# Optimization experiments

Hardware: AMD Instinct MI355X
Metric: run time of the kernel (lower is better)

## Reference

```python
import jax, jax.numpy as jnp
import numpy as np

S = 2048          # total tokens (single sequence)
H = 2560          # hidden size
NH = 8            # query heads
NKV = 4           # kv heads
D = 256           # head dim
EPS = 1e-6
SCALING = 256.0 ** -0.5          # query_pre_attn_scalar ** -0.5
WINDOW = 1024 - 1                # config.sliding_window - 1
ROPE_THETA = 10000.0             # rope_local_base_freq (sliding layer)


def setup_inputs() -> dict:
    key = jax.random.key(0)
    ks = jax.random.split(key, 5)
    hidden_states = jax.random.normal(ks[0], (S, H), dtype=jnp.float32)
    # RoPE tables (default rope type, HF convention: freqs duplicated along last dim)
    inv_freq = 1.0 / (ROPE_THETA ** (np.arange(0, D, 2, dtype=np.float32) / D))
    pos = np.arange(S, dtype=np.float32)
    freqs = np.outer(pos, inv_freq)                 # [S, D/2]
    emb = np.concatenate([freqs, freqs], axis=-1)   # [S, D]
    cos = jnp.asarray(np.cos(emb), dtype=jnp.float32)
    sin = jnp.asarray(np.sin(emb), dtype=jnp.float32)
    w_qkv = jax.random.normal(ks[1], (H, (NH + 2 * NKV) * D), dtype=jnp.float32) * (H ** -0.5)
    w_o = jax.random.normal(ks[2], (NH * D, H), dtype=jnp.float32) * ((NH * D) ** -0.5)
    q_norm_w = jax.random.normal(ks[3], (D,), dtype=jnp.float32) * 0.02
    k_norm_w = jax.random.normal(ks[4], (D,), dtype=jnp.float32) * 0.02
    return {"hidden_states": hidden_states, "cos": cos, "sin": sin,
            "w_qkv": w_qkv, "w_o": w_o, "q_norm_w": q_norm_w, "k_norm_w": k_norm_w}


def _rms_norm(x, w):
    # Gemma3RMSNorm: x * rsqrt(mean(x^2)+eps) * (1 + w), computed in fp32
    var = jnp.mean(jnp.square(x), axis=-1, keepdims=True)
    return x * jax.lax.rsqrt(var + EPS) * (1.0 + w)


def _rotate_half(x):
    x1, x2 = jnp.split(x, 2, axis=-1)
    return jnp.concatenate([-x2, x1], axis=-1)


def reference(hidden_states, cos, sin, w_qkv, w_o, q_norm_w, k_norm_w):
    qkv = hidden_states @ w_qkv                          # [S, (NH+2NKV)*D]
    q, k, v = jnp.split(qkv, [NH * D, (NH + NKV) * D], axis=-1)
    q = q.reshape(S, NH, D)
    k = k.reshape(S, NKV, D)
    v = v.reshape(S, NKV, D)

    # per-head QK RMSNorm
    q = _rms_norm(q, q_norm_w)
    k = _rms_norm(k, k_norm_w)

    # RoPE (cos/sin broadcast over heads)
    c = cos[:, None, :]
    s = sin[:, None, :]
    q = q * c + _rotate_half(q) * s
    k = k * c + _rotate_half(k) * s

    # GQA expand kv heads
    rep = NH // NKV
    k = jnp.repeat(k, rep, axis=1)                       # [S, NH, D]
    v = jnp.repeat(v, rep, axis=1)

    scores = jnp.einsum('snd,tnd->nst', q, k) * SCALING  # [NH, S, S]
    i = jnp.arange(S)[:, None]
    j = jnp.arange(S)[None, :]
    allowed = (j <= i) & (i - j <= WINDOW)               # causal sliding window
    scores = jnp.where(allowed[None], scores, jnp.finfo(scores.dtype).min)
    probs = jax.nn.softmax(scores, axis=-1)
    attn = jnp.einsum('nst,tnd->snd', probs, v)          # [S, NH, D]
    out = attn.reshape(S, NH * D) @ w_o                  # [S, H]
    return out
```

## Files before the change

### kernel.cpp

```cpp
#include <hip/hip_runtime.h>
#include <hip/hip_bf16.h>
#include <cstdint>
#include <cstddef>

#define S_LEN 2048
#define HID   2560
#define NHQ   8
#define QKV_N 4096
#define ATT_N 2048
#define WIN   1023
#define SCALE 0.0625f
#define NINF  -3.0e38f

typedef __attribute__((ext_vector_type(8))) short bf16x8;
typedef __attribute__((ext_vector_type(4))) float f32x4;

__device__ __forceinline__ unsigned bf_hi(float f) {
  unsigned u = __builtin_bit_cast(unsigned, f);
  return (u + 0x7FFFu + ((u >> 16) & 1u)) >> 16;
}
__device__ __forceinline__ float bf_to_f(unsigned h) {
  return __builtin_bit_cast(float, h << 16);
}
__device__ __forceinline__ void g2l16(const void* g, void* l) {
  __builtin_amdgcn_global_load_lds((const __attribute__((address_space(1))) void*)g,
                                   (__attribute__((address_space(3))) void*)l,
                                   16, 0, 0);
}

__global__ __launch_bounds__(256) void split_rows(const float* __restrict__ X,
                                                  unsigned short* __restrict__ Xh,
                                                  unsigned short* __restrict__ Xl) {
  const size_t i = ((size_t)blockIdx.x * 256 + threadIdx.x) * 8;
  const float4 v0 = *(const float4*)(X + i);
  const float4 v1 = *(const float4*)(X + i + 4);
  const float f[8] = {v0.x, v0.y, v0.z, v0.w, v1.x, v1.y, v1.z, v1.w};
  unsigned hw[4], lw[4];
  #pragma unroll
  for (int j = 0; j < 4; ++j) {
    const unsigned h0 = bf_hi(f[2 * j]), h1 = bf_hi(f[2 * j + 1]);
    const float r0 = f[2 * j] - bf_to_f(h0), r1 = f[2 * j + 1] - bf_to_f(h1);
    hw[j] = h0 | (h1 << 16);
    lw[j] = bf_hi(r0) | (bf_hi(r1) << 16);
  }
  *(uint4*)(Xh + i) = make_uint4(hw[0], hw[1], hw[2], hw[3]);
  *(uint4*)(Xl + i) = make_uint4(lw[0], lw[1], lw[2], lw[3]);
}

__global__ __launch_bounds__(256) void split_transpose(const float* __restrict__ W,
                                                       unsigned short* __restrict__ Th,
                                                       unsigned short* __restrict__ Tl,
                                                       int K, int N) {
  __shared__ float tile[32][33];
  const int tid = threadIdx.x;
  const int kt = blockIdx.y * 32, nt = blockIdx.x * 32;
  {
    const int r = tid >> 3, c = (tid & 7) * 4;
    const float4 v = *(const float4*)(W + (size_t)(kt + r) * N + nt + c);
    tile[r][c] = v.x; tile[r][c + 1] = v.y; tile[r][c + 2] = v.z; tile[r][c + 3] = v.w;
  }
  __syncthreads();
  const int nl = tid >> 3, k = (tid & 7) * 4;
  unsigned hw[2], lw[2];
  #pragma unroll
  for (int j = 0; j < 2; ++j) {
    const float f0 = tile[k + 2 * j][nl], f1 = tile[k + 2 * j + 1][nl];
    const unsigned h0 = bf_hi(f0), h1 = bf_hi(f1);
    const float r0 = f0 - bf_to_f(h0), r1 = f1 - bf_to_f(h1);
    hw[j] = h0 | (h1 << 16);
    lw[j] = bf_hi(r0) | (bf_hi(r1) << 16);
  }
  *(uint2*)(Th + (size_t)(nt + nl) * K + kt + k) = make_uint2(hw[0], hw[1]);
  *(uint2*)(Tl + (size_t)(nt + nl) * K + kt + k) = make_uint2(lw[0], lw[1]);
}

__global__ __launch_bounds__(256) void gemm_bf16_split(
    const unsigned short* __restrict__ Ah, const unsigned short* __restrict__ Al,
    const unsigned short* __restrict__ Bh, const unsigned short* __restrict__ Bl,
    float* __restrict__ C, int M, int N, int K, int nbx) {
  __shared__ __align__(16) unsigned short smem[16384];

  const int tid = threadIdx.x;
  int bid = blockIdx.x;
  const int cpx = gridDim.x >> 3;
  bid = (bid & 7) * cpx + (bid >> 3);
  const int bm = (bid / nbx) * 128;
  const int bn = (bid % nbx) * 128;

  const int lane = tid & 63;
  const int wv = tid >> 6;
  const int wr = (wv >> 1) * 64;
  const int wc = (wv & 1) * 64;
  const int frow = lane & 15;
  const int g16 = lane >> 4;

  const int u0 = tid, u1 = tid + 256;
  const int r0 = u0 >> 2, s0 = (u0 & 3) ^ ((r0 >> 1) & 3);
  const int r1 = u1 >> 2, s1 = (u1 & 3) ^ ((r1 >> 1) & 3);

  const unsigned short* a_h = Ah + (size_t)bm * K;
  const unsigned short* a_l = Al + (size_t)bm * K;
  const unsigned short* b_h = Bh + (size_t)bn * K;
  const unsigned short* b_l = Bl + (size_t)bn * K;

  unsigned short* d0 = smem + ((tid & ~63) << 3);
  unsigned short* d1 = smem + 2048 + ((tid & ~63) << 3);

  const int sx = (g16 ^ ((frow >> 1) & 3)) * 8;

  f32x4 acc[4][4] = {};

  for (int k0 = 0; k0 < K; k0 += 32) {
    __syncthreads();
    {
      const size_t o0 = (size_t)r0 * K + k0 + s0 * 8;
      const size_t o1 = (size_t)r1 * K + k0 + s1 * 8;
      g2l16(a_h + o0, d0);
      g2l16(a_h + o1, d1);
      g2l16(a_l + o0, d0 + 4096);
      g2l16(a_l + o1, d1 + 4096);
      g2l16(b_h + o0, d0 + 8192);
      g2l16(b_h + o1, d1 + 8192);
      g2l16(b_l + o0, d0 + 12288);
      g2l16(b_l + o1, d1 + 12288);
    }
    __syncthreads();

    bf16x8 ah[4], al[4], bh[4], bl[4];
    #pragma unroll
    for (int i = 0; i < 4; ++i) {
      ah[i] = *(const bf16x8*)&smem[(wr + i * 16 + frow) * 32 + sx];
      al[i] = *(const bf16x8*)&smem[4096 + (wr + i * 16 + frow) * 32 + sx];
      bh[i] = *(const bf16x8*)&smem[8192 + (wc + i * 16 + frow) * 32 + sx];
      bl[i] = *(const bf16x8*)&smem[12288 + (wc + i * 16 + frow) * 32 + sx];
    }
    #pragma unroll
    for (int i = 0; i < 4; ++i)
      #pragma unroll
      for (int j = 0; j < 4; ++j) {
        acc[i][j] = __builtin_amdgcn_mfma_f32_16x16x32_bf16(ah[i], bh[j], acc[i][j], 0, 0, 0);
        acc[i][j] = __builtin_amdgcn_mfma_f32_16x16x32_bf16(ah[i], bl[j], acc[i][j], 0, 0, 0);
        acc[i][j] = __builtin_amdgcn_mfma_f32_16x16x32_bf16(al[i], bh[j], acc[i][j], 0, 0, 0);
      }
  }

  #pragma unroll
  for (int i = 0; i < 4; ++i) {
    const int row0 = bm + wr + i * 16 + g16 * 4;
    #pragma unroll
    for (int j = 0; j < 4; ++j) {
      const int c = bn + wc + j * 16 + frow;
      #pragma unroll
      for (int r = 0; r < 4; ++r)
        C[(size_t)(row0 + r) * N + c] = acc[i][j][r];
    }
  }
}

__global__ __launch_bounds__(256) void qk_norm_rope_split(
    const float* __restrict__ qkv, const float* __restrict__ cosp,
    const float* __restrict__ sinp, const float* __restrict__ qw,
    const float* __restrict__ kw,
    unsigned short* __restrict__ Qh, unsigned short* __restrict__ Ql,
    unsigned short* __restrict__ Kh, unsigned short* __restrict__ Kl) {
  const int lane = threadIdx.x & 63;
  const int wave = threadIdx.x >> 6;
  const int row  = blockIdx.x * 4 + wave;
  const int s    = row / 12;
  const int c    = row % 12;
  const float* p = qkv + (size_t)s * QKV_N + c * 256;

  float4 x = *(const float4*)(p + lane * 4);
  float ss = x.x * x.x + x.y * x.y + x.z * x.z + x.w * x.w;
  #pragma unroll
  for (int off = 32; off; off >>= 1) ss += __shfl_xor(ss, off);
  const float scale = rsqrtf(ss * (1.0f / 256.0f) + 1e-6f);

  const float* wp = (c < 8) ? qw : kw;
  float4 w4 = *(const float4*)(wp + lane * 4);
  float y0 = x.x * scale * (1.0f + w4.x);
  float y1 = x.y * scale * (1.0f + w4.y);
  float y2 = x.z * scale * (1.0f + w4.z);
  float y3 = x.w * scale * (1.0f + w4.w);

  float z0 = __shfl_xor(y0, 32);
  float z1 = __shfl_xor(y1, 32);
  float z2 = __shfl_xor(y2, 32);
  float z3 = __shfl_xor(y3, 32);
  const float sgn = (lane < 32) ? -1.0f : 1.0f;

  float4 c4 = *(const float4*)(cosp + (size_t)s * 256 + lane * 4);
  float4 s4 = *(const float4*)(sinp + (size_t)s * 256 + lane * 4);
  float o[4];
  o[0] = y0 * c4.x + sgn * z0 * s4.x;
  o[1] = y1 * c4.y + sgn * z1 * s4.y;
  o[2] = y2 * c4.z + sgn * z2 * s4.z;
  o[3] = y3 * c4.w + sgn * z3 * s4.w;

  const float mul = (c < 8) ? SCALE : 1.0f;
  #pragma unroll
  for (int j = 0; j < 4; ++j) o[j] *= mul;

  unsigned h[4], lo[4];
  #pragma unroll
  for (int j = 0; j < 4; ++j) {
    h[j] = bf_hi(o[j]);
    lo[j] = bf_hi(o[j] - bf_to_f(h[j]));
  }
  const size_t off = ((c < 8) ? ((size_t)c * S_LEN + s)
                              : ((size_t)(c - 8) * S_LEN + s)) * 256 + lane * 4;
  unsigned short* dh = (c < 8 ? Qh : Kh) + off;
  unsigned short* dl = (c < 8 ? Ql : Kl) + off;
  *(uint2*)dh = make_uint2(h[0] | (h[1] << 16), h[2] | (h[3] << 16));
  *(uint2*)dl = make_uint2(lo[0] | (lo[1] << 16), lo[2] | (lo[3] << 16));
}

__global__ __launch_bounds__(256) void v_split_transpose(
    const float* __restrict__ qkv,
    unsigned short* __restrict__ VTh, unsigned short* __restrict__ VTl) {
  __shared__ float tile[32][33];
  const int tid = threadIdx.x;
  const int s0 = blockIdx.x * 32, d0 = blockIdx.y * 32, kvh = blockIdx.z;
  {
    const int r = tid >> 3, c = (tid & 7) * 4;
    const float4 v = *(const float4*)(qkv + (size_t)(s0 + r) * QKV_N + 3072 + kvh * 256 + d0 + c);
    tile[r][c] = v.x; tile[r][c + 1] = v.y; tile[r][c + 2] = v.z; tile[r][c + 3] = v.w;
  }
  __syncthreads();
  const int dd = tid >> 3, sc = (tid & 7) * 4;
  unsigned h[4], lo[4];
  #pragma unroll
  for (int j = 0; j < 4; ++j) {
    const float f = tile[sc + j][dd];
    h[j] = bf_hi(f);
    lo[j] = bf_hi(f - bf_to_f(h[j]));
  }
  const size_t off = ((size_t)kvh * 256 + d0 + dd) * S_LEN + s0 + sc;
  *(uint2*)(VTh + off) = make_uint2(h[0] | (h[1] << 16), h[2] | (h[3] << 16));
  *(uint2*)(VTl + off) = make_uint2(lo[0] | (lo[1] << 16), lo[2] | (lo[3] << 16));
}

#define PH_U  32768
#define PL_U  34048
__global__ __launch_bounds__(128, 2) void attn_mfma(
    const unsigned short* __restrict__ Qh, const unsigned short* __restrict__ Ql,
    const unsigned short* __restrict__ Kh, const unsigned short* __restrict__ Kl,
    const unsigned short* __restrict__ VTh, const unsigned short* __restrict__ VTl,
    unsigned short* __restrict__ Oh, unsigned short* __restrict__ Ol) {
  __shared__ __align__(16) unsigned short smem[35328];

  const int tid  = threadIdx.x;
  const int lane = tid & 63;
  const int wv   = __builtin_amdgcn_readfirstlane(tid >> 6);
  const int b    = blockIdx.x;
  const int xcd  = b & 7;
  const int kvh  = xcd >> 1;
  const int head = kvh * 2 + ((b >> 3) & 1);
  const int q0   = (((b >> 4) << 1) | (xcd & 1)) * 32;
  const int g16  = lane >> 4;
  const int c16  = lane & 15;

  const int qrow = q0 + wv * 16 + c16;
  bf16x8 qh[8], ql[8];
  {
    const unsigned short* qph = Qh + ((size_t)head * S_LEN + qrow) * 256 + g16 * 8;
    const unsigned short* qpl = Ql + ((size_t)head * S_LEN + qrow) * 256 + g16 * 8;
    #pragma unroll
    for (int dc = 0; dc < 8; ++dc) {
      qh[dc] = *(const bf16x8*)(qph + dc * 32);
      ql[dc] = *(const bf16x8*)(qpl + dc * 32);
    }
  }

  f32x4 o_acc[16] = {};
  float m_run[4], l_run[4];
  #pragma unroll
  for (int r = 0; r < 4; ++r) { m_run[r] = NINF; l_run[r] = 0.0f; }

  const int rmin = q0 + wv * 16, rmax = rmin + 15;
  const unsigned short* kh_g  = Kh  + (size_t)kvh * S_LEN * 256;
  const unsigned short* kl_g  = Kl  + (size_t)kvh * S_LEN * 256;
  const unsigned short* vth_g = VTh + (size_t)kvh * 256 * S_LEN;
  const unsigned short* vtl_g = VTl + (size_t)kvh * 256 * S_LEN;

  const int kstart = (q0 > WIN) ? ((q0 - WIN) & ~31) : 0;
  const int kend   = q0 + 31;

  for (int t0 = kstart; t0 <= kend; t0 += 32) {
    {
      char* lbase = (char*)smem + ((tid & ~63) << 4);
      #pragma unroll
      for (int i = 0; i < 8; ++i) {
        const int uu = i * 128 + tid, row = uu >> 5, sl = uu & 31;
        g2l16(kh_g + (size_t)(t0 + row) * 256 + ((sl ^ (row & 7)) * 8),
              lbase + i * 2048);
      }
      #pragma unroll
      for (int i = 0; i < 8; ++i) {
        const int uu = i * 128 + tid, row = uu >> 5, sl = uu & 31;
        g2l16(kl_g + (size_t)(t0 + row) * 256 + ((sl ^ (row & 7)) * 8),
              lbase + 16384 + i * 2048);
      }
      #pragma unroll
      for (int i = 0; i < 8; ++i) {
        const int uu = i * 128 + tid, d = uu >> 2, sl = uu & 3;
        g2l16(vth_g + (size_t)d * S_LEN + t0 + ((sl ^ ((d >> 1) & 3)) * 8),
              lbase + 32768 + i * 2048);
      }
      #pragma unroll
      for (int i = 0; i < 8; ++i) {
        const int uu = i * 128 + tid, d = uu >> 2, sl = uu & 3;
        g2l16(vtl_g + (size_t)d * S_LEN + t0 + ((sl ^ ((d >> 1) & 3)) * 8),
              lbase + 49152 + i * 2048);
      }
    }
    __syncthreads();

    const bool active = (t0 <= rmax) && (t0 + 31 + WIN >= rmin);
    if (active) {
      f32x4 sa[2] = {};
      #pragma unroll
      for (int t = 0; t < 2; ++t) {
        const int krow = t * 16 + c16;
        const int swz = krow & 7;
        #pragma unroll
        for (int dc = 0; dc < 8; ++dc) {
          const int sl = ((dc * 4 + g16) ^ swz) * 16;
          const bf16x8 kfh = *(const bf16x8*)((const char*)smem + krow * 512 + sl);
          const bf16x8 kfl = *(const bf16x8*)((const char*)smem + 16384 + krow * 512 + sl);
          sa[t] = __builtin_amdgcn_mfma_f32_16x16x32_bf16(qh[dc], kfh, sa[t], 0, 0, 0);
          sa[t] = __builtin_amdgcn_mfma_f32_16x16x32_bf16(qh[dc], kfl, sa[t], 0, 0, 0);
          sa[t] = __builtin_amdgcn_mfma_f32_16x16x32_bf16(ql[dc], kfh, sa[t], 0, 0, 0);
        }
      }

      const int k0c = t0 + c16;
      #pragma unroll
      for (int r = 0; r < 4; ++r) {
        const int q = rmin + g16 * 4 + r;
        const bool v0 = (k0c <= q) && (q - k0c <= WIN);
        const bool v1 = (k0c + 16 <= q) && (q - (k0c + 16) <= WIN);
        float s0 = v0 ? sa[0][r] : NINF;
        float s1 = v1 ? sa[1][r] : NINF;
        float mx = fmaxf(s0, s1);
        #pragma unroll
        for (int off = 8; off; off >>= 1) mx = fmaxf(mx, __shfl_xor(mx, off));
        const float m_new = fmaxf(m_run[r], mx);
        const float rs = __expf(m_run[r] - m_new);
        const float p0 = v0 ? __expf(s0 - m_new) : 0.0f;
        const float p1 = v1 ? __expf(s1 - m_new) : 0.0f;
        float psum = p0 + p1;
        #pragma unroll
        for (int off = 8; off; off >>= 1) psum += __shfl_xor(psum, off);
        l_run[r] = l_run[r] * rs + psum;
        m_run[r] = m_new;
        #pragma unroll
        for (int dt = 0; dt < 16; ++dt) o_acc[dt][r] *= rs;
        const int pro = wv * 640 + (g16 * 4 + r) * 40;
        const unsigned h0 = bf_hi(p0), h1 = bf_hi(p1);
        smem[PH_U + pro + c16]      = (unsigned short)h0;
        smem[PH_U + pro + 16 + c16] = (unsigned short)h1;
        smem[PL_U + pro + c16]      = (unsigned short)bf_hi(p0 - bf_to_f(h0));
        smem[PL_U + pro + 16 + c16] = (unsigned short)bf_hi(p1 - bf_to_f(h1));
      }

      const bf16x8 pah = *(const bf16x8*)&smem[PH_U + wv * 640 + c16 * 40 + g16 * 8];
      const bf16x8 pal = *(const bf16x8*)&smem[PL_U + wv * 640 + c16 * 40 + g16 * 8];
      #pragma unroll
      for (int dt = 0; dt < 16; ++dt) {
        const int vrow = dt * 16 + c16;
        const int sl = (g16 ^ ((vrow >> 1) & 3)) * 16;
        const bf16x8 vfh = *(const bf16x8*)((const char*)smem + 32768 + vrow * 64 + sl);
        const bf16x8 vfl = *(const bf16x8*)((const char*)smem + 49152 + vrow * 64 + sl);
        o_acc[dt] = __builtin_amdgcn_mfma_f32_16x16x32_bf16(pah, vfh, o_acc[dt], 0, 0, 0);
        o_acc[dt] = __builtin_amdgcn_mfma_f32_16x16x32_bf16(pah, vfl, o_acc[dt], 0, 0, 0);
        o_acc[dt] = __builtin_amdgcn_mfma_f32_16x16x32_bf16(pal, vfh, o_acc[dt], 0, 0, 0);
      }
    }
    __syncthreads();
  }

  #pragma unroll
  for (int r = 0; r < 4; ++r) {
    const float inv = 1.0f / l_run[r];
    const size_t rowo = (size_t)(rmin + g16 * 4 + r) * ATT_N + head * 256 + c16;
    #pragma unroll
    for (int dt = 0; dt < 16; ++dt) {
      const float o = o_acc[dt][r] * inv;
      const unsigned h = bf_hi(o);
      Oh[rowo + dt * 16] = (unsigned short)h;
      Ol[rowo + dt * 16] = (unsigned short)bf_hi(o - bf_to_f(h));
    }
  }
}

extern "C" void kernel_launch(void* const* d_in, const int* in_sizes, int n_in,
                              void* d_out, int out_size, void* d_ws, size_t ws_size,
                              hipStream_t stream) {
  const float* hs    = (const float*)d_in[0];
  const float* cosp  = (const float*)d_in[1];
  const float* sinp  = (const float*)d_in[2];
  const float* w_qkv = (const float*)d_in[3];
  const float* w_o   = (const float*)d_in[4];
  const float* qw    = (const float*)d_in[5];
  const float* kw    = (const float*)d_in[6];

  const size_t MB = 1024 * 1024;
  char* ws = (char*)d_ws;
  float* qkv = (float*)ws;
  unsigned short* wh = (unsigned short*)(ws + 32 * MB);
  unsigned short* wl = (unsigned short*)(ws + 52 * MB);
  unsigned short* Qh = (unsigned short*)(ws + 32 * MB);
  unsigned short* Ql = (unsigned short*)(ws + 40 * MB);
  unsigned short* Kh = (unsigned short*)(ws + 48 * MB);
  unsigned short* Kl = (unsigned short*)(ws + 52 * MB);
  unsigned short* VTh = (unsigned short*)(ws + 56 * MB);
  unsigned short* VTl = (unsigned short*)(ws + 60 * MB);
  unsigned short* Oh = (unsigned short*)ws;
  unsigned short* Ol = (unsigned short*)(ws + 8 * MB);
  unsigned short* oh = (unsigned short*)(ws + 16 * MB);
  unsigned short* ol = (unsigned short*)(ws + 26 * MB);
  unsigned short* Ahs = (unsigned short*)d_out;
  unsigned short* Als = Ahs + (size_t)S_LEN * HID;
  float* out = (float*)d_out;

  split_rows<<<(S_LEN * HID) / (256 * 8), 256, 0, stream>>>(hs, Ahs, Als);
  split_transpose<<<dim3(QKV_N / 32, HID / 32), 256, 0, stream>>>(
      w_qkv, wh, wl, HID, QKV_N);
  gemm_bf16_split<<<(S_LEN / 128) * (QKV_N / 128), 256, 0, stream>>>(
      Ahs, Als, wh, wl, qkv, S_LEN, QKV_N, HID, QKV_N / 128);
  qk_norm_rope_split<<<(S_LEN * 12) / 4, 256, 0, stream>>>(
      qkv, cosp, sinp, qw, kw, Qh, Ql, Kh, Kl);
  v_split_transpose<<<dim3(S_LEN / 32, 256 / 32, 4), 256, 0, stream>>>(
      qkv, VTh, VTl);
  attn_mfma<<<512, 128, 0, stream>>>(Qh, Ql, Kh, Kl, VTh, VTl, Oh, Ol);
  split_transpose<<<dim3(HID / 32, ATT_N / 32), 256, 0, stream>>>(
      w_o, oh, ol, ATT_N, HID);
  gemm_bf16_split<<<(S_LEN / 128) * (HID / 128), 256, 0, stream>>>(
      Oh, Ol, oh, ol, out, S_LEN, HID, ATT_N, HID / 128);
}
```

Measured before the change: 502.4 us.

## Split attention KV range in two partitions with a separate combine kernel

Attention is split into single-wave blocks of 16 query rows. Each block handles half of the key tiles for its query tile and writes unnormalised fp32 partial outputs plus running max and sum. A new combine kernel merges the two partials and emits the hi/lo bf16 split output. K and V fragments are now read straight from global memory instead of being staged through shared memory. This is meant to raise parallelism and remove block-wide barriers, at the cost of losing LDS reuse across waves, extra fp32 partial traffic and an extra kernel launch.

```diff
diff --git a/kernel.cpp b/kernel.cpp
--- a/kernel.cpp
+++ b/kernel.cpp
@@ -240,31 +240,29 @@
   *(uint2*)(VTl + off) = make_uint2(lo[0] | (lo[1] << 16), lo[2] | (lo[3] << 16));
 }
 
-#define PH_U  32768
-#define PL_U  34048
-__global__ __launch_bounds__(128, 2) void attn_mfma(
+__global__ __launch_bounds__(64, 2) void attn_part(
     const unsigned short* __restrict__ Qh, const unsigned short* __restrict__ Ql,
     const unsigned short* __restrict__ Kh, const unsigned short* __restrict__ Kl,
     const unsigned short* __restrict__ VTh, const unsigned short* __restrict__ VTl,
-    unsigned short* __restrict__ Oh, unsigned short* __restrict__ Ol) {
-  __shared__ __align__(16) unsigned short smem[35328];
-
-  const int tid  = threadIdx.x;
-  const int lane = tid & 63;
-  const int wv   = __builtin_amdgcn_readfirstlane(tid >> 6);
+    float* __restrict__ O0, float* __restrict__ O1, float* __restrict__ ML) {
+  __shared__ __align__(16) unsigned short smem[1280];
+
+  const int lane = threadIdx.x & 63;
   const int b    = blockIdx.x;
   const int xcd  = b & 7;
   const int kvh  = xcd >> 1;
   const int head = kvh * 2 + ((b >> 3) & 1);
-  const int q0   = (((b >> 4) << 1) | (xcd & 1)) * 32;
+  const int rest = b >> 4;
+  const int kh   = rest & 1;
+  const int qt   = ((rest >> 1) << 1) | (xcd & 1);
+  const int q0   = qt * 16;
   const int g16  = lane >> 4;
   const int c16  = lane & 15;
 
-  const int qrow = q0 + wv * 16 + c16;
   bf16x8 qh[8], ql[8];
   {
-    const unsigned short* qph = Qh + ((size_t)head * S_LEN + qrow) * 256 + g16 * 8;
-    const unsigned short* qpl = Ql + ((size_t)head * S_LEN + qrow) * 256 + g16 * 8;
+    const unsigned short* qph = Qh + ((size_t)head * S_LEN + q0 + c16) * 256 + g16 * 8;
+    const unsigned short* qpl = Ql + ((size_t)head * S_LEN + q0 + c16) * 256 + g16 * 8;
     #pragma unroll
     for (int dc = 0; dc < 8; ++dc) {
       qh[dc] = *(const bf16x8*)(qph + dc * 32);
@@ -277,121 +275,120 @@
   #pragma unroll
   for (int r = 0; r < 4; ++r) { m_run[r] = NINF; l_run[r] = 0.0f; }
 
-  const int rmin = q0 + wv * 16, rmax = rmin + 15;
   const unsigned short* kh_g  = Kh  + (size_t)kvh * S_LEN * 256;
   const unsigned short* kl_g  = Kl  + (size_t)kvh * S_LEN * 256;
   const unsigned short* vth_g = VTh + (size_t)kvh * 256 * S_LEN;
   const unsigned short* vtl_g = VTl + (size_t)kvh * 256 * S_LEN;
 
   const int kstart = (q0 > WIN) ? ((q0 - WIN) & ~31) : 0;
-  const int kend   = q0 + 31;
-
-  for (int t0 = kstart; t0 <= kend; t0 += 32) {
-    {
-      char* lbase = (char*)smem + ((tid & ~63) << 4);
-      #pragma unroll
-      for (int i = 0; i < 8; ++i) {
-        const int uu = i * 128 + tid, row = uu >> 5, sl = uu & 31;
-        g2l16(kh_g + (size_t)(t0 + row) * 256 + ((sl ^ (row & 7)) * 8),
-              lbase + i * 2048);
+  const int ntiles = ((q0 + 15 - kstart) >> 5) + 1;
+  const int n0 = (ntiles + 1) >> 1;
+  const int t_lo = kstart + (kh ? n0 * 32 : 0);
+  const int t_hi = kstart + (kh ? ntiles * 32 : n0 * 32);
+
+  for (int t0 = t_lo; t0 < t_hi; t0 += 32) {
+    f32x4 sa[2] = {};
+    #pragma unroll
+    for (int t = 0; t < 2; ++t) {
+      const unsigned short* kph = kh_g + (size_t)(t0 + t * 16 + c16) * 256 + g16 * 8;
+      const unsigned short* kpl = kl_g + (size_t)(t0 + t * 16 + c16) * 256 + g16 * 8;
+      #pragma unroll
+      for (int dc = 0; dc < 8; ++dc) {
+        const bf16x8 kfh = *(const bf16x8*)(kph + dc * 32);
+        const bf16x8 kfl = *(const bf16x8*)(kpl + dc * 32);
+        sa[t] = __builtin_amdgcn_mfma_f32_16x16x32_bf16(qh[dc], kfh, sa[t], 0, 0, 0);
+        sa[t] = __builtin_amdgcn_mfma_f32_16x16x32_bf16(qh[dc], kfl, sa[t], 0, 0, 0);
+        sa[t] = __builtin_amdgcn_mfma_f32_16x16x32_bf16(ql[dc], kfh, sa[t], 0, 0, 0);
       }
-      #pragma unroll
-      for (int i = 0; i < 8; ++i) {
-        const int uu = i * 128 + tid, row = uu >> 5, sl = uu & 31;
-        g2l16(kl_g + (size_t)(t0 + row) * 256 + ((sl ^ (row & 7)) * 8),
-              lbase + 16384 + i * 2048);
-      }
-      #pragma unroll
-      for (int i = 0; i < 8; ++i) {
-        const int uu = i * 128 + tid, d = uu >> 2, sl = uu & 3;
-        g2l16(vth_g + (size_t)d * S_LEN + t0 + ((sl ^ ((d >> 1) & 3)) * 8),
-              lbase + 32768 + i * 2048);
-      }
-      #pragma unroll
-      for (int i = 0; i < 8; ++i) {
-        const int uu = i * 128 + tid, d = uu >> 2, sl = uu & 3;
-        g2l16(vtl_g + (size_t)d * S_LEN + t0 + ((sl ^ ((d >> 1) & 3)) * 8),
-              lbase + 49152 + i * 2048);
-      }
-    }
-    __syncthreads();
-
-    const bool active = (t0 <= rmax) && (t0 + 31 + WIN >= rmin);
-    if (active) {
-      f32x4 sa[2] = {};
-      #pragma unroll
-      for (int t = 0; t < 2; ++t) {
-        const int krow = t * 16 + c16;
-        const int swz = krow & 7;
-        #pragma unroll
-        for (int dc = 0; dc < 8; ++dc) {
-          const int sl = ((dc * 4 + g16) ^ swz) * 16;
-          const bf16x8 kfh = *(const bf16x8*)((const char*)smem + krow * 512 + sl);
-          const bf16x8 kfl = *(const bf16x8*)((const char*)smem + 16384 + krow * 512 + sl);
-          sa[t] = __builtin_amdgcn_mfma_f32_16x16x32_bf16(qh[dc], kfh, sa[t], 0, 0, 0);
-          sa[t] = __builtin_amdgcn_mfma_f32_16x16x32_bf16(qh[dc], kfl, sa[t], 0, 0, 0);
-          sa[t] = __builtin_amdgcn_mfma_f32_16x16x32_bf16(ql[dc], kfh, sa[t], 0, 0, 0);
-        }
-      }
-
-      const int k0c = t0 + c16;
-      #pragma unroll
-      for (int r = 0; r < 4; ++r) {
-        const int q = rmin + g16 * 4 + r;
-        const bool v0 = (k0c <= q) && (q - k0c <= WIN);
-        const bool v1 = (k0c + 16 <= q) && (q - (k0c + 16) <= WIN);
-        float s0 = v0 ? sa[0][r] : NINF;
-        float s1 = v1 ? sa[1][r] : NINF;
-        float mx = fmaxf(s0, s1);
-        #pragma unroll
-        for (int off = 8; off; off >>= 1) mx = fmaxf(mx, __shfl_xor(mx, off));
-        const float m_new = fmaxf(m_run[r], mx);
-        const float rs = __expf(m_run[r] - m_new);
-        const float p0 = v0 ? __expf(s0 - m_new) : 0.0f;
-        const float p1 = v1 ? __expf(s1 - m_new) : 0.0f;
-        float psum = p0 + p1;
-        #pragma unroll
-        for (int off = 8; off; off >>= 1) psum += __shfl_xor(psum, off);
-        l_run[r] = l_run[r] * rs + psum;
-        m_run[r] = m_new;
-        #pragma unroll
-        for (int dt = 0; dt < 16; ++dt) o_acc[dt][r] *= rs;
-        const int pro = wv * 640 + (g16 * 4 + r) * 40;
-        const unsigned h0 = bf_hi(p0), h1 = bf_hi(p1);
-        smem[PH_U + pro + c16]      = (unsigned short)h0;
-        smem[PH_U + pro + 16 + c16] = (unsigned short)h1;
-        smem[PL_U + pro + c16]      = (unsigned short)bf_hi(p0 - bf_to_f(h0));
-        smem[PL_U + pro + 16 + c16] = (unsigned short)bf_hi(p1 - bf_to_f(h1));
-      }
-
-      const bf16x8 pah = *(const bf16x8*)&smem[PH_U + wv * 640 + c16 * 40 + g16 * 8];
-      const bf16x8 pal = *(const bf16x8*)&smem[PL_U + wv * 640 + c16 * 40 + g16 * 8];
-      #pragma unroll
-      for (int dt = 0; dt < 16; ++dt) {
-        const int vrow = dt * 16 + c16;
-        const int sl = (g16 ^ ((vrow >> 1) & 3)) * 16;
-        const bf16x8 vfh = *(const bf16x8*)((const char*)smem + 32768 + vrow * 64 + sl);
-        const bf16x8 vfl = *(const bf16x8*)((const char*)smem + 49152 + vrow * 64 + sl);
-        o_acc[dt] = __builtin_amdgcn_mfma_f32_16x16x32_bf16(pah, vfh, o_acc[dt], 0, 0, 0);
-        o_acc[dt] = __builtin_amdgcn_mfma_f32_16x16x32_bf16(pah, vfl, o_acc[dt], 0, 0, 0);
-        o_acc[dt] = __builtin_amdgcn_mfma_f32_16x16x32_bf16(pal, vfh, o_acc[dt], 0, 0, 0);
-      }
-    }
-    __syncthreads();
-  }
-
+    }
+
+    const int k0c = t0 + c16;
+    #pragma unroll
+    for (int r = 0; r < 4; ++r) {
+      const int q = q0 + g16 * 4 + r;
+      const bool v0 = (k0c <= q) && (q - k0c <= WIN);
+      const bool v1 = (k0c + 16 <= q) && (q - (k0c + 16) <= WIN);
+      float s0 = v0 ? sa[0][r] : NINF;
+      float s1 = v1 ? sa[1][r] : NINF;
+      float mx = fmaxf(s0, s1);
+      #pragma unroll
+      for (int off = 8; off; off >>= 1) mx = fmaxf(mx, __shfl_xor(mx, off));
+      const float m_new = fmaxf(m_run[r], mx);
+      const float rs = __expf(m_run[r] - m_new);
+      const float p0 = v0 ? __expf(s0 - m_new) : 0.0f;
+      const float p1 = v1 ? __expf(s1 - m_new) : 0.0f;
+      float psum = p0 + p1;
+      #pragma unroll
+      for (int off = 8; off; off >>= 1) psum += __shfl_xor(psum, off);
+      l_run[r] = l_run[r] * rs + psum;
+      m_run[r] = m_new;
+      #pragma unroll
+      for (int dt = 0; dt < 16; ++dt) o_acc[dt][r] *= rs;
+      const int pro = (g16 * 4 + r) * 40;
+      const unsigned h0 = bf_hi(p0), h1 = bf_hi(p1);
+      smem[pro + c16]       = (unsigned short)h0;
+      smem[pro + 16 + c16]  = (unsigned short)h1;
+      smem[640 + pro + c16]      = (unsigned short)bf_hi(p0 - bf_to_f(h0));
+      smem[640 + pro + 16 + c16] = (unsigned short)bf_hi(p1 - bf_to_f(h1));
+    }
+
+    const bf16x8 pah = *(const bf16x8*)&smem[c16 * 40 + g16 * 8];
+    const bf16x8 pal = *(const bf16x8*)&smem[640 + c16 * 40 + g16 * 8];
+    #pragma unroll
+    for (int dt = 0; dt < 16; ++dt) {
+      const bf16x8 vfh = *(const bf16x8*)(vth_g + (size_t)(dt * 16 + c16) * S_LEN + t0 + g16 * 8);
+      const bf16x8 vfl = *(const bf16x8*)(vtl_g + (size_t)(dt * 16 + c16) * S_LEN + t0 + g16 * 8);
+      o_acc[dt] = __builtin_amdgcn_mfma_f32_16x16x32_bf16(pah, vfh, o_acc[dt], 0, 0, 0);
+      o_acc[dt] = __builtin_amdgcn_mfma_f32_16x16x32_bf16(pah, vfl, o_acc[dt], 0, 0, 0);
+      o_acc[dt] = __builtin_amdgcn_mfma_f32_16x16x32_bf16(pal, vfh, o_acc[dt], 0, 0, 0);
+    }
+  }
+
+  float* op = (kh ? O1 : O0) + ((size_t)head * S_LEN + q0) * 256;
   #pragma unroll
   for (int r = 0; r < 4; ++r) {
-    const float inv = 1.0f / l_run[r];
-    const size_t rowo = (size_t)(rmin + g16 * 4 + r) * ATT_N + head * 256 + c16;
-    #pragma unroll
-    for (int dt = 0; dt < 16; ++dt) {
-      const float o = o_acc[dt][r] * inv;
-      const unsigned h = bf_hi(o);
-      Oh[rowo + dt * 16] = (unsigned short)h;
-      Ol[rowo + dt * 16] = (unsigned short)bf_hi(o - bf_to_f(h));
-    }
-  }
+    const int qloc = g16 * 4 + r;
+    #pragma unroll
+    for (int dt = 0; dt < 16; ++dt)
+      op[(size_t)qloc * 256 + dt * 16 + c16] = o_acc[dt][r];
+  }
+  if (c16 == 0) {
+    float* mlb = ML + kh * 32768;
+    #pragma unroll
+    for (int r = 0; r < 4; ++r) {
+      const int q = q0 + g16 * 4 + r;
+      mlb[head * S_LEN + q]         = m_run[r];
+      mlb[16384 + head * S_LEN + q] = l_run[r];
+    }
+  }
+}
+
+__global__ __launch_bounds__(256) void attn_combine(
+    const float* __restrict__ O0, const float* __restrict__ O1,
+    const float* __restrict__ ML,
+    unsigned short* __restrict__ Oh, unsigned short* __restrict__ Ol) {
+  const int lane = threadIdx.x & 63;
+  const int wave = threadIdx.x >> 6;
+  const int row  = blockIdx.x * 4 + wave;
+  const int head = row >> 11, s = row & 2047;
+  const float m0 = ML[row],         l0 = ML[16384 + row];
+  const float m1 = ML[32768 + row], l1 = ML[49152 + row];
+  const float m  = fmaxf(m0, m1);
+  const float w0 = __expf(m0 - m), w1 = __expf(m1 - m);
+  const float inv = 1.0f / (l0 * w0 + l1 * w1);
+  const float4 a = *(const float4*)(O0 + (size_t)row * 256 + lane * 4);
+  const float4 bq = *(const float4*)(O1 + (size_t)row * 256 + lane * 4);
+  float o[4] = {(a.x * w0 + bq.x * w1) * inv, (a.y * w0 + bq.y * w1) * inv,
+                (a.z * w0 + bq.z * w1) * inv, (a.w * w0 + bq.w * w1) * inv};
+  unsigned h[4], lo[4];
+  #pragma unroll
+  for (int j = 0; j < 4; ++j) {
+    h[j] = bf_hi(o[j]);
+    lo[j] = bf_hi(o[j] - bf_to_f(h[j]));
+  }
+  const size_t rowo = (size_t)s * ATT_N + head * 256 + lane * 4;
+  *(uint2*)(Oh + rowo) = make_uint2(h[0] | (h[1] << 16), h[2] | (h[3] << 16));
+  *(uint2*)(Ol + rowo) = make_uint2(lo[0] | (lo[1] << 16), lo[2] | (lo[3] << 16));
 }
 
 extern "C" void kernel_launch(void* const* d_in, const int* in_sizes, int n_in,
@@ -416,12 +413,15 @@
   unsigned short* Kl = (unsigned short*)(ws + 52 * MB);
   unsigned short* VTh = (unsigned short*)(ws + 56 * MB);
   unsigned short* VTl = (unsigned short*)(ws + 60 * MB);
-  unsigned short* Oh = (unsigned short*)ws;
-  unsigned short* Ol = (unsigned short*)(ws + 8 * MB);
-  unsigned short* oh = (unsigned short*)(ws + 16 * MB);
-  unsigned short* ol = (unsigned short*)(ws + 26 * MB);
+  float* O0 = (float*)ws;
+  float* MLp = (float*)(ws + 16 * MB);
+  unsigned short* Oh = (unsigned short*)(ws + 32 * MB);
+  unsigned short* Ol = (unsigned short*)(ws + 40 * MB);
+  unsigned short* oh = (unsigned short*)(ws + 48 * MB);
+  unsigned short* ol = (unsigned short*)(ws + 58 * MB);
   unsigned short* Ahs = (unsigned short*)d_out;
   unsigned short* Als = Ahs + (size_t)S_LEN * HID;
+  float* O1 = (float*)d_out;
   float* out = (float*)d_out;
 
   split_rows<<<(S_LEN * HID) / (256 * 8), 256, 0, stream>>>(hs, Ahs, Als);
@@ -433,7 +433,8 @@
       qkv, cosp, sinp, qw, kw, Qh, Ql, Kh, Kl);
   v_split_transpose<<<dim3(S_LEN / 32, 256 / 32, 4), 256, 0, stream>>>(
       qkv, VTh, VTl);
-  attn_mfma<<<512, 128, 0, stream>>>(Qh, Ql, Kh, Kl, VTh, VTl, Oh, Ol);
+  attn_part<<<2048, 64, 0, stream>>>(Qh, Ql, Kh, Kl, VTh, VTl, O0, O1, MLp);
+  attn_combine<<<(S_LEN * NHQ) / 4, 256, 0, stream>>>(O0, O1, MLp, Oh, Ol);
   split_transpose<<<dim3(HID / 32, ATT_N / 32), 256, 0, stream>>>(
       w_o, oh, ol, ATT_N, HID);
   gemm_bf16_split<<<(S_LEN / 128) * (HID / 128), 256, 0, stream>>>(
```

Measured after the change: 574.6 us. +14.4%, slower.
